# Kernel optimization log

Hardware: AMD Instinct MI355X
Metric: run time of the kernel (lower is better)

Reference implementation:

```python
import jax, jax.numpy as jnp
import numpy as np

B, N, L, H = 32, 1024, 512, 8  # batch, num_id, Input_len, num_head
EPS = 1e-5


def _ln(x, g, b):
    m = jnp.mean(x, axis=-1, keepdims=True)
    v = jnp.mean((x - m) ** 2, axis=-1, keepdims=True)
    return (x - m) / jnp.sqrt(v + EPS) * g + b


def setup_inputs() -> dict:
    key = jax.random.key(0)
    ks = iter(jax.random.split(key, 40))
    w = lambda shape, s=0.02: jax.random.normal(next(ks), shape, jnp.float32) * s
    inp = {"x": jax.random.normal(next(ks), (B, N, L), jnp.float32)}
    for p in ("t", "c"):  # Time_de_att and cross_de_att params (conv1d k=1 -> [L,L])
        inp[f"{p}_Wq"] = w((L, L)); inp[f"{p}_bq"] = w((L,))
        inp[f"{p}_Wk"] = w((L, L)); inp[f"{p}_bk"] = w((L,))
        inp[f"{p}_Wv"] = w((L, L)); inp[f"{p}_bv"] = w((L,))
        inp[f"{p}_Wo"] = w((L, L, 1, H)); inp[f"{p}_bo"] = w((L,))  # Conv2d kernel (1,H)
        inp[f"{p}_g"] = jnp.ones((L,), jnp.float32); inp[f"{p}_b"] = jnp.zeros((L,), jnp.float32)
    inp["s_Wq"] = w((N, N)); inp["s_bq"] = w((N,))
    inp["s_Wk"] = w((N, N)); inp["s_bk"] = w((N,))
    inp["s_Wv"] = w((N, N)); inp["s_bv"] = w((N,))
    inp["s_W1"] = w((1, H)); inp["s_b1"] = w((1,))
    return inp


def _conv1x1(x_cn, W, b):  # x_cn: [B,C,len], W: [O,C]
    return jnp.einsum('oc,bcn->bon', W, x_cn) + b[None, :, None]


def _de_att(xq_src, xkv_src, Wq, bq, Wk, bk, Wv, bv, Wo, bo, g, bt):
    # xq_src, xkv_src: [B,L,N] (channels-first, as after x.transpose(-2,-1))
    q = _conv1x1(xq_src, Wq, bq).transpose(0, 2, 1)   # [B,N,L]
    k = _conv1x1(xkv_src, Wk, bk)                     # [B,L,N]
    v = _conv1x1(xkv_src, Wv, bv).transpose(0, 2, 1)  # [B,N,L]
    kd = jnp.sqrt(jnp.float32(N) / H)                 # k.shape[-1] == num_id
    attn = jax.nn.softmax(jnp.matmul(q, k) / kd, axis=-1)  # [B,N,N]
    line = jnp.matmul(attn, v)                        # [B,N,L]
    # eval-mode: all heads identical -> Conv2d(1,H) combine == sum weights over head axis
    Wsum = Wo[:, :, 0, :].sum(-1)                     # [L,L]
    res = jnp.einsum('oc,bcn->bon', Wsum, line.transpose(0, 2, 1)) + bo[None, :, None]
    out = (xkv_src + res).transpose(0, 2, 1)          # [B,N,L]
    return _ln(out, g, bt)


def reference(x,
              t_Wq, t_bq, t_Wk, t_bk, t_Wv, t_bv, t_Wo, t_bo, t_g, t_b,
              c_Wq, c_bq, c_Wk, c_bk, c_Wv, c_bv, c_Wo, c_bo, c_g, c_b,
              s_Wq, s_bq, s_Wk, s_bk, s_Wv, s_bv, s_W1, s_b1):
    xt = x.transpose(0, 2, 1)  # [B,L,N]
    # Time_de_att (self-attention over nodes, time as channels)
    time_out = _de_att(xt, xt, t_Wq, t_bq, t_Wk, t_bk, t_Wv, t_bv, t_Wo, t_bo, t_g, t_b)  # [B,N,L]
    # space_att2 (attention over time, nodes as features)
    q = xt @ s_Wq.T + s_bq                          # [B,L,N]
    k = (xt @ s_Wk.T + s_bk).transpose(0, 2, 1)     # [B,N,L]
    v = xt @ s_Wv.T + s_bv                          # [B,L,N]
    kd = jnp.sqrt(jnp.float32(L) / H)               # k.shape[-1] == Input_len
    line = jnp.matmul(jax.nn.softmax(jnp.matmul(q, k) / kd, axis=-1), v)  # [B,L,N]
    space_out = (line * s_W1.sum() + s_b1[0]).transpose(0, 2, 1)          # [B,N,L]
    # cross_de_att: q from space_out, k/v + residual from time_out
    out = _de_att(space_out.transpose(0, 2, 1), time_out.transpose(0, 2, 1),
                  c_Wq, c_bq, c_Wk, c_bk, c_Wv, c_bv, c_Wo, c_bo, c_g, c_b)
    return out  # [B,N,L]
```

## Files before the change

kernel.cpp:

```cpp
#include <hip/hip_runtime.h>
#include <hip/hip_bf16.h>

typedef __bf16 bf16;
typedef __bf16 bf16x8 __attribute__((ext_vector_type(8)));
typedef __bf16 bf16x4 __attribute__((ext_vector_type(4)));
typedef __bf16 bf16x2 __attribute__((ext_vector_type(2)));
typedef float f32x4 __attribute__((ext_vector_type(4)));

#define BATCH 32
#define N_ID 1024
#define L_IN 512

static const long ACT_E = (long)BATCH * N_ID * L_IN;
static const long S_NL  = (long)N_ID * L_IN;
static const long S_TT  = (long)N_ID * N_ID;

__device__ __forceinline__ void gload16(const bf16* g, bf16* l)
{
    __builtin_amdgcn_global_load_lds((__attribute__((address_space(1))) void*)g,
                                     (__attribute__((address_space(3))) void*)l, 16, 0, 0);
}

#define VM8 asm volatile("s_waitcnt vmcnt(8)" ::: "memory")
#define VM4 asm volatile("s_waitcnt vmcnt(4)" ::: "memory")
#define VM0 asm volatile("s_waitcnt vmcnt(0)" ::: "memory")
#define BAR __builtin_amdgcn_s_barrier()

#define COMPUTE(CIDX) \
    { \
      const bf16* pa = ldsb + (CIDX) * 8192; \
      const bf16* pb = pa + 4096; \
      bf16x8 af[4], bfv[4]; \
_Pragma("unroll") \
      for (int i = 0; i < 4; ++i) \
        af[i] = *(const bf16x8*)(pa + (wm * 64 + i * 16 + fr) * 32 + slotk); \
_Pragma("unroll") \
      for (int j = 0; j < 4; ++j) \
        bfv[j] = *(const bf16x8*)(pb + (wn * 64 + j * 16 + fr) * 32 + slotk); \
      __builtin_amdgcn_s_setprio(1); \
_Pragma("unroll") \
      for (int i = 0; i < 4; ++i) \
_Pragma("unroll") \
        for (int j = 0; j < 4; ++j) \
          acc[i][j] = __builtin_amdgcn_mfma_f32_16x16x32_bf16(af[i], bfv[j], acc[i][j], 0, 0, 0); \
      __builtin_amdgcn_s_setprio(0); \
    }

#define STAGE(CIDX, KT) { stg(ldsb + (CIDX) * 8192, Ab, lda, m0, KT); \
                          stg(ldsb + (CIDX) * 8192 + 4096, Bb, ldb, n0, KT); }

template<int EPI>
__global__ __launch_bounds__(256, 3)
void gemm3(const bf16* __restrict__ A, const bf16* __restrict__ Bm, void* __restrict__ Cout,
           const float* __restrict__ biasCol, const float* __restrict__ biasRow,
           const void* __restrict__ Res, const float* __restrict__ scal2,
           float scale, int K,
           long lda, long ldb, long ldc,
           long sA, long sB, long sC, long sRes, long sBR,
           unsigned gy, unsigned gxy, unsigned nwg)
{
    __shared__ __align__(16) bf16 ldsbuf[3 * 2 * 4096];
    bf16* ldsb = ldsbuf;

    unsigned id = blockIdx.x;
    {
        const unsigned q = nwg >> 3, r = nwg & 7;
        const unsigned xcd = id & 7, off = id >> 3;
        id = (xcd < r ? xcd * (q + 1) : r * (q + 1) + (xcd - r) * q) + off;
    }
    const unsigned bz = id / gxy;
    const unsigned rem = id - bz * gxy;
    const unsigned bx = rem / gy;
    const unsigned by = rem - bx * gy;

    const int t = threadIdx.x;
    const int w = t >> 6;
    const int lane = t & 63;
    const int fr = lane & 15;
    const int kg = lane >> 4;
    const int wm = w >> 1, wn = w & 1;
    const long z = bz;
    const long m0 = (long)bx * 128;
    const long n0 = (long)by * 128;
    const bf16* Ab = A + z * sA;
    const bf16* Bb = Bm + z * sB;

    const int srow = w * 16 + (lane >> 2);
    const int gc = (lane & 3) ^ ((lane >> 3) & 3);
    const int slotk = (kg ^ ((fr >> 1) & 3)) * 8;

    auto stg = [&](bf16* dst, const bf16* base, long ld, long rc0, int kt) {
#pragma unroll
        for (int r = 0; r < 2; ++r) {
            const int row = r * 64 + srow;
            const bf16* src = base + (rc0 + row) * ld + kt * 32 + gc * 8;
            gload16(src, dst + row * 32 + (lane & 3) * 8);
        }
    };

    f32x4 acc[4][4] = {};

    const int NT = K >> 5;
    STAGE(0, 0); STAGE(1, 1); STAGE(2, 2);

    int c = 0;
    for (int kt = 0; kt < NT - 2; ++kt) {
        VM8; BAR;
        COMPUTE(c);
        BAR;
        if (kt + 3 < NT) STAGE(c, kt + 3);
        c = (c == 2) ? 0 : c + 1;
    }
    VM4; BAR;
    COMPUTE(c);
    BAR;
    c = (c == 2) ? 0 : c + 1;
    VM0; BAR;
    COMPUTE(c);

    float e0 = 0.f, e1 = 0.f;
    if constexpr (EPI == 8) { e0 = scal2[0]; e1 = scal2[1]; }

    float rs[16];
    if constexpr (EPI == 6) {
#pragma unroll
        for (int vv = 0; vv < 16; ++vv) rs[vv] = 0.f;
    }

#pragma unroll
    for (int i = 0; i < 4; ++i) {
        const long rb = m0 + wm * 64 + i * 16 + kg * 4;
        float rin[4];
        if constexpr (EPI == 7) {
#pragma unroll
            for (int r = 0; r < 4; ++r) rin[r] = 1.f / biasRow[z * sBR + rb + r];
        }
#pragma unroll
        for (int j = 0; j < 4; ++j) {
            const long cc = n0 + wn * 64 + j * 16 + fr;
            float cinv = 0.f, vj = 0.f;
            if constexpr (EPI == 8) cinv = 1.f / biasCol[z * sBR + cc];
            if constexpr (EPI == 6) vj = biasCol[z * sBR + cc];
#pragma unroll
            for (int r = 0; r < 4; ++r) {
                const long rr = rb + r;
                const float v = acc[i][j][r];
                const long idx = z * sC + rr * ldc + cc;
                if constexpr (EPI == 1)      ((bf16*)Cout)[idx] = (bf16)(v + biasRow[rr]);
                else if constexpr (EPI == 3) ((bf16*)Cout)[idx] = (bf16)v;
                else if constexpr (EPI == 6) {
                    const float e = __builtin_amdgcn_exp2f(v * scale + vj);
                    ((bf16*)Cout)[idx] = (bf16)e;
                    rs[i * 4 + r] += e;
                }
                else if constexpr (EPI == 7) ((bf16*)Cout)[idx] =
                    (bf16)(v * rin[r]
                           + (float)((const bf16*)Res)[z * sRes + rr * ldc + cc] + biasCol[cc]);
                else                  ((bf16*)Cout)[idx] = (bf16)(v * cinv * e0 + e1);
            }
        }
    }

    if constexpr (EPI == 6) {
#pragma unroll
        for (int vv = 0; vv < 16; ++vv) {
            rs[vv] += __shfl_xor(rs[vv], 1);
            rs[vv] += __shfl_xor(rs[vv], 2);
            rs[vv] += __shfl_xor(rs[vv], 4);
            rs[vv] += __shfl_xor(rs[vv], 8);
        }
        if (fr == 0) {
            float* Rs = (float*)biasRow + z * sBR;
#pragma unroll
            for (int i = 0; i < 4; ++i)
#pragma unroll
                for (int r = 0; r < 4; ++r) {
                    const long rr = m0 + wm * 64 + i * 16 + kg * 4 + r;
                    atomicAdd(Rs + rr, rs[i * 4 + r]);
                }
        }
    }
}

template<int OUTBF>
__global__ __launch_bounds__(128)
void ln_rows(const bf16* __restrict__ X, const float* __restrict__ g,
             const float* __restrict__ bta, void* __restrict__ out)
{
    const long row = blockIdx.x;
    const int t = threadIdx.x;
    bf16x4 b4 = *(const bf16x4*)(X + row * 512 + t * 4);
    float v[4] = { (float)b4[0], (float)b4[1], (float)b4[2], (float)b4[3] };
    float s1 = v[0] + v[1] + v[2] + v[3];
    float s2 = v[0]*v[0] + v[1]*v[1] + v[2]*v[2] + v[3]*v[3];
#pragma unroll
    for (int o = 32; o > 0; o >>= 1) { s1 += __shfl_xor(s1, o); s2 += __shfl_xor(s2, o); }
    __shared__ float r1[2], r2[2];
    const int w = t >> 6, l = t & 63;
    if (l == 0) { r1[w] = s1; r2[w] = s2; }
    __syncthreads();
    s1 = r1[0] + r1[1];
    s2 = r2[0] + r2[1];
    const float mean = s1 * (1.f / 512.f);
    const float var  = s2 * (1.f / 512.f) - mean * mean;
    const float rstd = rsqrtf(var + 1e-5f);
    const int c = t * 4;
    if constexpr (OUTBF) {
        bf16x4 o4;
#pragma unroll
        for (int k = 0; k < 4; ++k) o4[k] = (bf16)((v[k] - mean) * rstd * g[c + k] + bta[c + k]);
        *(bf16x4*)((bf16*)out + row * 512 + c) = o4;
    } else {
        f32x4 o4;
#pragma unroll
        for (int k = 0; k < 4; ++k) o4[k] = (v[k] - mean) * rstd * g[c + k] + bta[c + k];
        *(f32x4*)((float*)out + row * 512 + c) = o4;
    }
}

__global__ __launch_bounds__(256)
void transpose_cvt(const float* __restrict__ x, bf16* __restrict__ Xb, bf16* __restrict__ xt)
{
    __shared__ bf16 tile[32][33];
    const int b = blockIdx.z;
    const int n0 = blockIdx.x * 32, l0 = blockIdx.y * 32;
    const long base = (long)b * N_ID * L_IN;
    const int tx = threadIdx.x, ty = threadIdx.y;
#pragma unroll
    for (int i = ty; i < 32; i += 8) {
        const long idx = base + (long)(n0 + i) * L_IN + l0 + tx;
        const bf16 s = (bf16)x[idx];
        Xb[idx] = s;
        tile[i][tx] = s;
    }
    __syncthreads();
#pragma unroll
    for (int i = ty; i < 32; i += 8)
        xt[base + (long)(l0 + i) * N_ID + n0 + tx] = tile[tx][i];
}

template<int N>
__global__ __launch_bounds__(256)
void transpose_mat(const float* __restrict__ a, const float* __restrict__ b,
                   bf16* __restrict__ da, bf16* __restrict__ db)
{
    __shared__ bf16 tile[32][33];
    const float* src = blockIdx.z ? b : a;
    bf16* dst = blockIdx.z ? db : da;
    const int c0 = blockIdx.x * 32, r0 = blockIdx.y * 32;
    const int tx = threadIdx.x, ty = threadIdx.y;
#pragma unroll
    for (int i = ty; i < 32; i += 8)
        tile[i][tx] = (bf16)src[(long)(r0 + i) * N + c0 + tx];
    __syncthreads();
#pragma unroll
    for (int i = ty; i < 32; i += 8)
        dst[(long)(c0 + i) * N + r0 + tx] = tile[tx][i];
}

__global__ void cvt_one(const float* __restrict__ s, bf16* __restrict__ d, int n)
{
    const int i = (blockIdx.x * 256 + threadIdx.x) * 4;
    if (i < n) {
        f32x4 v = *(const f32x4*)(s + i);
        bf16x4 o; o[0] = (bf16)v[0]; o[1] = (bf16)v[1]; o[2] = (bf16)v[2]; o[3] = (bf16)v[3];
        *(bf16x4*)(d + i) = o;
    }
}

__global__ void wo_sum2(const float* __restrict__ a, const float* __restrict__ b,
                        bf16* __restrict__ da, bf16* __restrict__ db)
{
    const int i = blockIdx.x * 256 + threadIdx.x;
    const float* src = blockIdx.y ? b : a;
    bf16* dst = blockIdx.y ? db : da;
    const float* p = src + (long)i * 8;
    float s = 0.f;
#pragma unroll
    for (int h = 0; h < 8; ++h) s += p[h];
    dst[i] = (bf16)s;
}

__global__ __launch_bounds__(64)
void biasfold2(const bf16* __restrict__ WsA, const float* __restrict__ bvA, const float* __restrict__ boA, float* __restrict__ outA,
               const bf16* __restrict__ WsB, const float* __restrict__ bvB, const float* __restrict__ boB, float* __restrict__ outB)
{
    const bf16* Ws = blockIdx.y ? WsB : WsA;
    const float* bv = blockIdx.y ? bvB : bvA;
    const float* bo = blockIdx.y ? boB : boA;
    float* out = blockIdx.y ? outB : outA;
    const int o = blockIdx.x;
    float s = 0.f;
    for (int l = threadIdx.x; l < 512; l += 64)
        s += (float)Ws[(long)o * 512 + l] * bv[l];
#pragma unroll
    for (int off = 32; off > 0; off >>= 1) s += __shfl_xor(s, off);
    if (threadIdx.x == 0) out[o] = bo[o] + s;
}

__global__ __launch_bounds__(64)
void vbarfold(const bf16* WkTrT, const float* tbq, float* vbarT,
              const bf16* WkTrC, const float* cbq, float* vbarC,
              const bf16* sWkTr, const float* sbq, float* vbarS,
              const float* sW1, const float* sb1, float* scal)
{
    const int o = blockIdx.x;
    const int y = blockIdx.y;
    if (y == 3) {
        if (o == 0 && threadIdx.x == 0) {
            float s = 0.f;
            for (int h = 0; h < 8; ++h) s += sW1[h];
            scal[0] = s; scal[1] = sb1[0];
        }
        return;
    }
    const bf16* W; const float* b; float* out; int D;
    if (y == 0)      { if (o >= 512) return; W = WkTrT; b = tbq; out = vbarT; D = 512; }
    else if (y == 1) { if (o >= 512) return; W = WkTrC; b = cbq; out = vbarC; D = 512; }
    else             { W = sWkTr; b = sbq; out = vbarS; D = 1024; }
    float s = 0.f;
    for (int a = threadIdx.x; a < D; a += 64)
        s += (float)W[(long)o * D + a] * b[a];
#pragma unroll
    for (int off = 32; off > 0; off >>= 1) s += __shfl_xor(s, off);
    if (threadIdx.x == 0) out[o] = s;
}

template<int D>
__global__ __launch_bounds__(256)
void vrow(const bf16* __restrict__ Src, const float* __restrict__ vbar,
          float* __restrict__ out, float scale2)
{
    const long row = (long)blockIdx.x * 4 + (threadIdx.x >> 6);
    const int lane = threadIdx.x & 63;
    const bf16* r = Src + row * D;
    float s = 0.f;
#pragma unroll
    for (int u = 0; u < D / 512; ++u) {
        bf16x8 xv = *(const bf16x8*)(r + u * 512 + lane * 8);
        const float* vb = vbar + u * 512 + lane * 8;
#pragma unroll
        for (int e = 0; e < 8; ++e) s += (float)xv[e] * vb[e];
    }
#pragma unroll
    for (int o = 32; o > 0; o >>= 1) s += __shfl_xor(s, o);
    if (lane == 0) out[row] = s * scale2;
}

static void launch_gemm(int epi, const bf16* A, const bf16* B, void* C,
                        const float* bc, const float* br, const void* res, const float* sc2,
                        float scale, int M, int N, int K,
                        long lda, long ldb, long ldc,
                        long sA, long sB, long sC, long sRes, long sBR,
                        int batches, hipStream_t st)
{
    const unsigned gx = M / 128, gy = N / 128;
    const unsigned gxy = gx * gy, nwg = gxy * (unsigned)batches;
    dim3 g(nwg), blk(256);
    switch (epi) {
    case 1: gemm3<1><<<g, blk, 0, st>>>(A, B, C, bc, br, res, sc2, scale, K, lda, ldb, ldc, sA, sB, sC, sRes, sBR, gy, gxy, nwg); break;
    case 3: gemm3<3><<<g, blk, 0, st>>>(A, B, C, bc, br, res, sc2, scale, K, lda, ldb, ldc, sA, sB, sC, sRes, sBR, gy, gxy, nwg); break;
    case 6: gemm3<6><<<g, blk, 0, st>>>(A, B, C, bc, br, res, sc2, scale, K, lda, ldb, ldc, sA, sB, sC, sRes, sBR, gy, gxy, nwg); break;
    case 7: gemm3<7><<<g, blk, 0, st>>>(A, B, C, bc, br, res, sc2, scale, K, lda, ldb, ldc, sA, sB, sC, sRes, sBR, gy, gxy, nwg); break;
    default: gemm3<8><<<g, blk, 0, st>>>(A, B, C, bc, br, res, sc2, scale, K, lda, ldb, ldc, sA, sB, sC, sRes, sBR, gy, gxy, nwg); break;
    }
}

extern "C" void kernel_launch(void* const* d_in, const int* in_sizes, int n_in,
                              void* d_out, int out_size, void* d_ws, size_t ws_size,
                              hipStream_t stream)
{
    (void)in_sizes; (void)n_in; (void)out_size;

    const float* x   = (const float*)d_in[0];
    const float* tWq = (const float*)d_in[1];  const float* tbq = (const float*)d_in[2];
    const float* tWk = (const float*)d_in[3];  const float* tbk = (const float*)d_in[4];
    const float* tWv = (const float*)d_in[5];  const float* tbv = (const float*)d_in[6];
    const float* tWo = (const float*)d_in[7];  const float* tbo = (const float*)d_in[8];
    const float* tg  = (const float*)d_in[9];  const float* tb  = (const float*)d_in[10];
    const float* cWq = (const float*)d_in[11]; const float* cbq = (const float*)d_in[12];
    const float* cWk = (const float*)d_in[13]; const float* cbk = (const float*)d_in[14];
    const float* cWv = (const float*)d_in[15]; const float* cbv = (const float*)d_in[16];
    const float* cWo = (const float*)d_in[17]; const float* cbo = (const float*)d_in[18];
    const float* cg  = (const float*)d_in[19]; const float* cb  = (const float*)d_in[20];
    const float* sWq = (const float*)d_in[21]; const float* sbq = (const float*)d_in[22];
    const float* sWk = (const float*)d_in[23]; const float* sbk = (const float*)d_in[24];
    const float* sWv = (const float*)d_in[25]; const float* sbv = (const float*)d_in[26];
    const float* sW1 = (const float*)d_in[27]; const float* sb1 = (const float*)d_in[28];
    (void)tbk; (void)cbk; (void)sbk;

    char* p = (char*)d_ws;
    auto alloc = [&](size_t bytes) -> char* {
        char* r = p; p += (bytes + 255) & ~(size_t)255; return r;
    };

    bf16* WsT   = (bf16*)alloc(262144 * 2);
    bf16* WsC   = (bf16*)alloc(262144 * 2);
    bf16* WkTrT = (bf16*)alloc(262144 * 2);
    bf16* WkTrC = (bf16*)alloc(262144 * 2);
    bf16* WvTrT = (bf16*)alloc(262144 * 2);
    bf16* WvTrC = (bf16*)alloc(262144 * 2);
    bf16* WqTrT = (bf16*)alloc(262144 * 2);
    bf16* WqTrC = (bf16*)alloc(262144 * 2);
    bf16* WvWT  = (bf16*)alloc(262144 * 2);
    bf16* WvWC  = (bf16*)alloc(262144 * 2);
    bf16* MTt   = (bf16*)alloc(262144 * 2);
    bf16* MTc   = (bf16*)alloc(262144 * 2);
    bf16* sWqTr = (bf16*)alloc(1048576 * 2);
    bf16* sWkTr = (bf16*)alloc(1048576 * 2);
    bf16* MTs   = (bf16*)alloc(1048576 * 2);
    bf16* WvS   = (bf16*)alloc(1048576 * 2);
    float* scal  = (float*)alloc(256);
    float* biasT = (float*)alloc(512 * 4);
    float* biasC = (float*)alloc(512 * 4);
    float* vbarT = (float*)alloc(512 * 4);
    float* vbarC = (float*)alloc(512 * 4);
    float* vbarS = (float*)alloc(1024 * 4);

    const size_t ACT_B = (size_t)ACT_E * 2;
    bf16* bufG = (bf16*)alloc(ACT_B);
    bf16* Xb   = (bf16*)alloc(ACT_B);
    bf16* TO   = (bf16*)alloc(ACT_B);
    bf16* xt   = (bf16*)alloc(ACT_B);
    bf16* bufV = (bf16*)alloc(ACT_B);
    bf16* PL   = (bf16*)alloc(ACT_B);
    float* vpre = (float*)alloc(BATCH * 1024 * 4);
    float* Rbuf = (float*)alloc(BATCH * 1024 * 4);

    size_t used = (size_t)(p - (char*)d_ws);
    int CB = 32;
    while (CB > 1 && used + (size_t)CB * 2097152ULL + 4096 > ws_size) CB >>= 1;
    bf16* Sbuf = (bf16*)alloc((size_t)CB * 2097152ULL);
    bf16* Pbuf = Sbuf;

    const float L2E = 1.4426950408889634f;
    const float rsc_t2 = 0.08838834764831845f * L2E;
    const float rsc_s2 = 0.125f * L2E;

    transpose_mat<512><<<dim3(16, 16, 2), dim3(32, 8), 0, stream>>>(tWv, cWv, WvTrT, WvTrC);
    transpose_mat<512><<<dim3(16, 16, 2), dim3(32, 8), 0, stream>>>(tWq, cWq, WqTrT, WqTrC);
    transpose_mat<512><<<dim3(16, 16, 2), dim3(32, 8), 0, stream>>>(tWk, cWk, WkTrT, WkTrC);
    transpose_mat<1024><<<dim3(32, 32, 2), dim3(32, 8), 0, stream>>>(sWq, sWk, sWqTr, sWkTr);
    cvt_one<<<dim3(1024), dim3(256), 0, stream>>>(sWv, WvS, 1048576);
    wo_sum2<<<dim3(1024, 2), dim3(256), 0, stream>>>(tWo, cWo, WsT, WsC);
    biasfold2<<<dim3(512, 2), dim3(64), 0, stream>>>(WsT, tbv, tbo, biasT, WsC, cbv, cbo, biasC);
    vbarfold<<<dim3(1024, 4), dim3(64), 0, stream>>>(WkTrT, tbq, vbarT, WkTrC, cbq, vbarC,
                                                     sWkTr, sbq, vbarS, sW1, sb1, scal);
    launch_gemm(3, WsT, WvTrT, WvWT, nullptr, nullptr, nullptr, nullptr, 0.f,
                512, 512, 512, 512, 512, 512, 262144, 262144, 262144, 0, 0, 4, stream);
    launch_gemm(3, sWkTr, sWqTr, MTs, nullptr, nullptr, nullptr, nullptr, 0.f,
                1024, 1024, 1024, 1024, 1024, 1024, 0, 0, 0, 0, 0, 1, stream);
    transpose_cvt<<<dim3(32, 16, BATCH), dim3(32, 8), 0, stream>>>(x, Xb, xt);

    auto attn_tc = [&](const bf16* Kb, const bf16* ResP, const float* biasP) {
        for (int c0 = 0; c0 < BATCH; c0 += CB) {
            const long off = (long)c0 * S_NL;
            hipMemsetAsync(Rbuf, 0, (size_t)CB * 1024 * 4, stream);
            launch_gemm(6, bufG + off, Kb + off, Sbuf, vpre + (long)c0 * 1024, Rbuf, nullptr, nullptr, rsc_t2,
                        1024, 1024, 512, 512, 512, 1024, S_NL, S_NL, S_TT, 0, 1024, CB, stream);
            launch_gemm(7, Pbuf, bufV + off, PL + off, biasP, Rbuf, ResP + off, nullptr, 0.f,
                        1024, 512, 1024, 1024, 1024, 512, S_TT, S_NL, S_NL, S_NL, 1024, CB, stream);
        }
    };

    launch_gemm(3, Xb, MTt, bufG, nullptr, nullptr, nullptr, nullptr, 0.f,
                32768, 512, 512, 512, 512, 512, 0, 0, 0, 0, 0, 1, stream);
    launch_gemm(3, WvWT, Xb, bufV, nullptr, nullptr, nullptr, nullptr, 0.f,
                512, 1024, 512, 512, 512, 1024, 0, S_NL, S_NL, 0, 0, BATCH, stream);
    vrow<512><<<dim3(8192), dim3(256), 0, stream>>>(Xb, vbarT, vpre, rsc_t2);
    attn_tc(Xb, Xb, biasT);
    ln_rows<1><<<dim3(32768), dim3(128), 0, stream>>>(PL, tg, tb, TO);

    bf16* SOp = Xb;
    launch_gemm(3, xt, MTs, bufG, nullptr, nullptr, nullptr, nullptr, 0.f,
                16384, 1024, 1024, 1024, 1024, 1024, 0, 0, 0, 0, 0, 1, stream);
    launch_gemm(1, WvS, xt, bufV, nullptr, sbv, nullptr, nullptr, 0.f,
                1024, 512, 1024, 1024, 1024, 512, 0, S_NL, S_NL, 0, 0, BATCH, stream);
    vrow<1024><<<dim3(4096), dim3(256), 0, stream>>>(xt, vbarS, vpre, rsc_s2);
    for (int c0 = 0; c0 < BATCH; c0 += CB) {
        const long off = (long)c0 * S_NL;
        hipMemsetAsync(Rbuf, 0, (size_t)CB * 512 * 4, stream);
        launch_gemm(6, bufG + off, xt + off, Sbuf, vpre + (long)c0 * 512, Rbuf, nullptr, nullptr, rsc_s2,
                    512, 512, 1024, 1024, 1024, 512, S_NL, S_NL, (long)L_IN * L_IN, 0, 512, CB, stream);
        launch_gemm(8, bufV + off, Pbuf, SOp + off, Rbuf, nullptr, nullptr, scal, 0.f,
                    1024, 512, 512, 512, 512, 512, S_NL, (long)L_IN * L_IN, S_NL, 0, 512, CB, stream);
    }

    launch_gemm(3, Xb, MTc, bufG, nullptr, nullptr, nullptr, nullptr, 0.f,
                32768, 512, 512, 512, 512, 512, 0, 0, 0, 0, 0, 1, stream);
    launch_gemm(3, WvWC, TO, bufV, nullptr, nullptr, nullptr, nullptr, 0.f,
                512, 1024, 512, 512, 512, 1024, 0, S_NL, S_NL, 0, 0, BATCH, stream);
    vrow<512><<<dim3(8192), dim3(256), 0, stream>>>(TO, vbarC, vpre, rsc_t2);
    attn_tc(TO, TO, biasC);
    ln_rows<0><<<dim3(32768), dim3(128), 0, stream>>>(PL, cg, cb, d_out);
}
```

Baseline: 649.9 us.

## Double-buffer GEMM for occupancy, replace atomic row sums with slot partials, batch small kernels

The GEMM pipeline drops from three LDS stages to two so that four workgroups can fit per CU instead of three. The softmax row-sum accumulation now writes per-tile partial sums into slot buffers instead of using atomics, and the consumer epilogues reduce those slots. This removes the memsets and atomic contention. The three weight transposes are merged into one launch, and LayerNorm now handles two rows per block. The shallower pipeline exposes more memory latency per workgroup, and the consumers do extra loads to reduce the partials.

```diff
diff --git a/kernel.cpp b/kernel.cpp
--- a/kernel.cpp
+++ b/kernel.cpp
@@ -21,7 +21,6 @@
                                      (__attribute__((address_space(3))) void*)l, 16, 0, 0);
 }
 
-#define VM8 asm volatile("s_waitcnt vmcnt(8)" ::: "memory")
 #define VM4 asm volatile("s_waitcnt vmcnt(4)" ::: "memory")
 #define VM0 asm volatile("s_waitcnt vmcnt(0)" ::: "memory")
 #define BAR __builtin_amdgcn_s_barrier()
@@ -50,16 +49,16 @@
                           stg(ldsb + (CIDX) * 8192 + 4096, Bb, ldb, n0, KT); }
 
 template<int EPI>
-__global__ __launch_bounds__(256, 3)
+__global__ __launch_bounds__(256, 4)
 void gemm3(const bf16* __restrict__ A, const bf16* __restrict__ Bm, void* __restrict__ Cout,
            const float* __restrict__ biasCol, const float* __restrict__ biasRow,
            const void* __restrict__ Res, const float* __restrict__ scal2,
            float scale, int K,
            long lda, long ldb, long ldc,
-           long sA, long sB, long sC, long sRes, long sBR,
+           long sA, long sB, long sC, long sRes, long sBR, long sVp, int nsl,
            unsigned gy, unsigned gxy, unsigned nwg)
 {
-    __shared__ __align__(16) bf16 ldsbuf[3 * 2 * 4096];
+    __shared__ __align__(16) bf16 ldsbuf[2 * 2 * 4096];
     bf16* ldsb = ldsbuf;
 
     unsigned id = blockIdx.x;
@@ -101,22 +100,16 @@
     f32x4 acc[4][4] = {};
 
     const int NT = K >> 5;
-    STAGE(0, 0); STAGE(1, 1); STAGE(2, 2);
-
-    int c = 0;
-    for (int kt = 0; kt < NT - 2; ++kt) {
-        VM8; BAR;
-        COMPUTE(c);
+    STAGE(0, 0); STAGE(1, 1);
+
+    for (int kt = 0; kt < NT - 1; ++kt) {
+        VM4; BAR;
+        COMPUTE(kt & 1);
         BAR;
-        if (kt + 3 < NT) STAGE(c, kt + 3);
-        c = (c == 2) ? 0 : c + 1;
-    }
-    VM4; BAR;
-    COMPUTE(c);
-    BAR;
-    c = (c == 2) ? 0 : c + 1;
+        if (kt + 2 < NT) STAGE(kt & 1, kt + 2);
+    }
     VM0; BAR;
-    COMPUTE(c);
+    COMPUTE((NT - 1) & 1);
 
     float e0 = 0.f, e1 = 0.f;
     if constexpr (EPI == 8) { e0 = scal2[0]; e1 = scal2[1]; }
@@ -133,14 +126,24 @@
         float rin[4];
         if constexpr (EPI == 7) {
 #pragma unroll
-            for (int r = 0; r < 4; ++r) rin[r] = 1.f / biasRow[z * sBR + rb + r];
+            for (int r = 0; r < 4; ++r) {
+                float s = biasRow[z * sBR + (rb + r) * 16 + fr];
+                s += __shfl_xor(s, 1); s += __shfl_xor(s, 2);
+                s += __shfl_xor(s, 4); s += __shfl_xor(s, 8);
+                rin[r] = 1.f / s;
+            }
         }
 #pragma unroll
         for (int j = 0; j < 4; ++j) {
             const long cc = n0 + wn * 64 + j * 16 + fr;
             float cinv = 0.f, vj = 0.f;
-            if constexpr (EPI == 8) cinv = 1.f / biasCol[z * sBR + cc];
-            if constexpr (EPI == 6) vj = biasCol[z * sBR + cc];
+            if constexpr (EPI == 8) {
+                float s = 0.f;
+#pragma unroll
+                for (int k8 = 0; k8 < 8; ++k8) s += biasCol[z * sBR + cc * 8 + k8];
+                cinv = 1.f / s;
+            }
+            if constexpr (EPI == 6) vj = biasCol[z * sVp + cc];
 #pragma unroll
             for (int r = 0; r < 4; ++r) {
                 const long rr = rb + r;
@@ -171,40 +174,42 @@
         }
         if (fr == 0) {
             float* Rs = (float*)biasRow + z * sBR;
+            const int slot = (int)by * 2 + wn;
 #pragma unroll
             for (int i = 0; i < 4; ++i)
 #pragma unroll
                 for (int r = 0; r < 4; ++r) {
                     const long rr = m0 + wm * 64 + i * 16 + kg * 4 + r;
-                    atomicAdd(Rs + rr, rs[i * 4 + r]);
+                    Rs[rr * nsl + slot] = rs[i * 4 + r];
                 }
         }
     }
 }
 
 template<int OUTBF>
-__global__ __launch_bounds__(128)
+__global__ __launch_bounds__(256)
 void ln_rows(const bf16* __restrict__ X, const float* __restrict__ g,
              const float* __restrict__ bta, void* __restrict__ out)
 {
-    const long row = blockIdx.x;
-    const int t = threadIdx.x;
-    bf16x4 b4 = *(const bf16x4*)(X + row * 512 + t * 4);
+    const int rloc = threadIdx.x >> 7;
+    const int t2 = threadIdx.x & 127;
+    const long row = (long)blockIdx.x * 2 + rloc;
+    bf16x4 b4 = *(const bf16x4*)(X + row * 512 + t2 * 4);
     float v[4] = { (float)b4[0], (float)b4[1], (float)b4[2], (float)b4[3] };
     float s1 = v[0] + v[1] + v[2] + v[3];
     float s2 = v[0]*v[0] + v[1]*v[1] + v[2]*v[2] + v[3]*v[3];
 #pragma unroll
     for (int o = 32; o > 0; o >>= 1) { s1 += __shfl_xor(s1, o); s2 += __shfl_xor(s2, o); }
-    __shared__ float r1[2], r2[2];
-    const int w = t >> 6, l = t & 63;
-    if (l == 0) { r1[w] = s1; r2[w] = s2; }
+    __shared__ float r1[2][2], r2[2][2];
+    const int w = t2 >> 6, l = t2 & 63;
+    if (l == 0) { r1[rloc][w] = s1; r2[rloc][w] = s2; }
     __syncthreads();
-    s1 = r1[0] + r1[1];
-    s2 = r2[0] + r2[1];
+    s1 = r1[rloc][0] + r1[rloc][1];
+    s2 = r2[rloc][0] + r2[rloc][1];
     const float mean = s1 * (1.f / 512.f);
     const float var  = s2 * (1.f / 512.f) - mean * mean;
     const float rstd = rsqrtf(var + 1e-5f);
-    const int c = t * 4;
+    const int c = t2 * 4;
     if constexpr (OUTBF) {
         bf16x4 o4;
 #pragma unroll
@@ -237,6 +242,25 @@
 #pragma unroll
     for (int i = ty; i < 32; i += 8)
         xt[base + (long)(l0 + i) * N_ID + n0 + tx] = tile[tx][i];
+}
+
+struct T6 { const float* s[6]; bf16* d[6]; };
+
+__global__ __launch_bounds__(256)
+void transpose512_6(T6 p)
+{
+    __shared__ bf16 tile[32][33];
+    const float* src = p.s[blockIdx.z];
+    bf16* dst = p.d[blockIdx.z];
+    const int c0 = blockIdx.x * 32, r0 = blockIdx.y * 32;
+    const int tx = threadIdx.x, ty = threadIdx.y;
+#pragma unroll
+    for (int i = ty; i < 32; i += 8)
+        tile[i][tx] = (bf16)src[(long)(r0 + i) * 512 + c0 + tx];
+    __syncthreads();
+#pragma unroll
+    for (int i = ty; i < 32; i += 8)
+        dst[(long)(c0 + i) * 512 + r0 + tx] = tile[tx][i];
 }
 
 template<int N>
@@ -351,18 +375,18 @@
                         const float* bc, const float* br, const void* res, const float* sc2,
                         float scale, int M, int N, int K,
                         long lda, long ldb, long ldc,
-                        long sA, long sB, long sC, long sRes, long sBR,
+                        long sA, long sB, long sC, long sRes, long sBR, long sVp, int nsl,
                         int batches, hipStream_t st)
 {
     const unsigned gx = M / 128, gy = N / 128;
     const unsigned gxy = gx * gy, nwg = gxy * (unsigned)batches;
     dim3 g(nwg), blk(256);
     switch (epi) {
-    case 1: gemm3<1><<<g, blk, 0, st>>>(A, B, C, bc, br, res, sc2, scale, K, lda, ldb, ldc, sA, sB, sC, sRes, sBR, gy, gxy, nwg); break;
-    case 3: gemm3<3><<<g, blk, 0, st>>>(A, B, C, bc, br, res, sc2, scale, K, lda, ldb, ldc, sA, sB, sC, sRes, sBR, gy, gxy, nwg); break;
-    case 6: gemm3<6><<<g, blk, 0, st>>>(A, B, C, bc, br, res, sc2, scale, K, lda, ldb, ldc, sA, sB, sC, sRes, sBR, gy, gxy, nwg); break;
-    case 7: gemm3<7><<<g, blk, 0, st>>>(A, B, C, bc, br, res, sc2, scale, K, lda, ldb, ldc, sA, sB, sC, sRes, sBR, gy, gxy, nwg); break;
-    default: gemm3<8><<<g, blk, 0, st>>>(A, B, C, bc, br, res, sc2, scale, K, lda, ldb, ldc, sA, sB, sC, sRes, sBR, gy, gxy, nwg); break;
+    case 1: gemm3<1><<<g, blk, 0, st>>>(A, B, C, bc, br, res, sc2, scale, K, lda, ldb, ldc, sA, sB, sC, sRes, sBR, sVp, nsl, gy, gxy, nwg); break;
+    case 3: gemm3<3><<<g, blk, 0, st>>>(A, B, C, bc, br, res, sc2, scale, K, lda, ldb, ldc, sA, sB, sC, sRes, sBR, sVp, nsl, gy, gxy, nwg); break;
+    case 6: gemm3<6><<<g, blk, 0, st>>>(A, B, C, bc, br, res, sc2, scale, K, lda, ldb, ldc, sA, sB, sC, sRes, sBR, sVp, nsl, gy, gxy, nwg); break;
+    case 7: gemm3<7><<<g, blk, 0, st>>>(A, B, C, bc, br, res, sc2, scale, K, lda, ldb, ldc, sA, sB, sC, sRes, sBR, sVp, nsl, gy, gxy, nwg); break;
+    default: gemm3<8><<<g, blk, 0, st>>>(A, B, C, bc, br, res, sc2, scale, K, lda, ldb, ldc, sA, sB, sC, sRes, sBR, sVp, nsl, gy, gxy, nwg); break;
     }
 }
 
@@ -374,20 +398,19 @@
 
     const float* x   = (const float*)d_in[0];
     const float* tWq = (const float*)d_in[1];  const float* tbq = (const float*)d_in[2];
-    const float* tWk = (const float*)d_in[3];  const float* tbk = (const float*)d_in[4];
+    const float* tWk = (const float*)d_in[3];
     const float* tWv = (const float*)d_in[5];  const float* tbv = (const float*)d_in[6];
     const float* tWo = (const float*)d_in[7];  const float* tbo = (const float*)d_in[8];
     const float* tg  = (const float*)d_in[9];  const float* tb  = (const float*)d_in[10];
     const float* cWq = (const float*)d_in[11]; const float* cbq = (const float*)d_in[12];
-    const float* cWk = (const float*)d_in[13]; const float* cbk = (const float*)d_in[14];
+    const float* cWk = (const float*)d_in[13];
     const float* cWv = (const float*)d_in[15]; const float* cbv = (const float*)d_in[16];
     const float* cWo = (const float*)d_in[17]; const float* cbo = (const float*)d_in[18];
     const float* cg  = (const float*)d_in[19]; const float* cb  = (const float*)d_in[20];
     const float* sWq = (const float*)d_in[21]; const float* sbq = (const float*)d_in[22];
-    const float* sWk = (const float*)d_in[23]; const float* sbk = (const float*)d_in[24];
+    const float* sWk = (const float*)d_in[23];
     const float* sWv = (const float*)d_in[25]; const float* sbv = (const float*)d_in[26];
     const float* sW1 = (const float*)d_in[27]; const float* sb1 = (const float*)d_in[28];
-    (void)tbk; (void)cbk; (void)sbk;
 
     char* p = (char*)d_ws;
     auto alloc = [&](size_t bytes) -> char* {
@@ -425,7 +448,7 @@
     bf16* bufV = (bf16*)alloc(ACT_B);
     bf16* PL   = (bf16*)alloc(ACT_B);
     float* vpre = (float*)alloc(BATCH * 1024 * 4);
-    float* Rbuf = (float*)alloc(BATCH * 1024 * 4);
+    float* Rbuf = (float*)alloc((size_t)BATCH * 1024 * 16 * 4);
 
     size_t used = (size_t)(p - (char*)d_ws);
     int CB = 32;
@@ -437,9 +460,10 @@
     const float rsc_t2 = 0.08838834764831845f * L2E;
     const float rsc_s2 = 0.125f * L2E;
 
-    transpose_mat<512><<<dim3(16, 16, 2), dim3(32, 8), 0, stream>>>(tWv, cWv, WvTrT, WvTrC);
-    transpose_mat<512><<<dim3(16, 16, 2), dim3(32, 8), 0, stream>>>(tWq, cWq, WqTrT, WqTrC);
-    transpose_mat<512><<<dim3(16, 16, 2), dim3(32, 8), 0, stream>>>(tWk, cWk, WkTrT, WkTrC);
+    T6 tj;
+    tj.s[0] = tWv; tj.s[1] = cWv; tj.s[2] = tWq; tj.s[3] = cWq; tj.s[4] = tWk; tj.s[5] = cWk;
+    tj.d[0] = WvTrT; tj.d[1] = WvTrC; tj.d[2] = WqTrT; tj.d[3] = WqTrC; tj.d[4] = WkTrT; tj.d[5] = WkTrC;
+    transpose512_6<<<dim3(16, 16, 6), dim3(32, 8), 0, stream>>>(tj);
     transpose_mat<1024><<<dim3(32, 32, 2), dim3(32, 8), 0, stream>>>(sWq, sWk, sWqTr, sWkTr);
     cvt_one<<<dim3(1024), dim3(256), 0, stream>>>(sWv, WvS, 1048576);
     wo_sum2<<<dim3(1024, 2), dim3(256), 0, stream>>>(tWo, cWo, WsT, WsC);
@@ -447,50 +471,48 @@
     vbarfold<<<dim3(1024, 4), dim3(64), 0, stream>>>(WkTrT, tbq, vbarT, WkTrC, cbq, vbarC,
                                                      sWkTr, sbq, vbarS, sW1, sb1, scal);
     launch_gemm(3, WsT, WvTrT, WvWT, nullptr, nullptr, nullptr, nullptr, 0.f,
-                512, 512, 512, 512, 512, 512, 262144, 262144, 262144, 0, 0, 4, stream);
+                512, 512, 512, 512, 512, 512, 262144, 262144, 262144, 0, 0, 0, 0, 4, stream);
     launch_gemm(3, sWkTr, sWqTr, MTs, nullptr, nullptr, nullptr, nullptr, 0.f,
-                1024, 1024, 1024, 1024, 1024, 1024, 0, 0, 0, 0, 0, 1, stream);
+                1024, 1024, 1024, 1024, 1024, 1024, 0, 0, 0, 0, 0, 0, 0, 1, stream);
     transpose_cvt<<<dim3(32, 16, BATCH), dim3(32, 8), 0, stream>>>(x, Xb, xt);
 
     auto attn_tc = [&](const bf16* Kb, const bf16* ResP, const float* biasP) {
         for (int c0 = 0; c0 < BATCH; c0 += CB) {
             const long off = (long)c0 * S_NL;
-            hipMemsetAsync(Rbuf, 0, (size_t)CB * 1024 * 4, stream);
             launch_gemm(6, bufG + off, Kb + off, Sbuf, vpre + (long)c0 * 1024, Rbuf, nullptr, nullptr, rsc_t2,
-                        1024, 1024, 512, 512, 512, 1024, S_NL, S_NL, S_TT, 0, 1024, CB, stream);
+                        1024, 1024, 512, 512, 512, 1024, S_NL, S_NL, S_TT, 0, 16384, 1024, 16, CB, stream);
             launch_gemm(7, Pbuf, bufV + off, PL + off, biasP, Rbuf, ResP + off, nullptr, 0.f,
-                        1024, 512, 1024, 1024, 1024, 512, S_TT, S_NL, S_NL, S_NL, 1024, CB, stream);
+                        1024, 512, 1024, 1024, 1024, 512, S_TT, S_NL, S_NL, S_NL, 16384, 0, 16, CB, stream);
         }
     };
 
     launch_gemm(3, Xb, MTt, bufG, nullptr, nullptr, nullptr, nullptr, 0.f,
-                32768, 512, 512, 512, 512, 512, 0, 0, 0, 0, 0, 1, stream);
+                32768, 512, 512, 512, 512, 512, 0, 0, 0, 0, 0, 0, 0, 1, stream);
     launch_gemm(3, WvWT, Xb, bufV, nullptr, nullptr, nullptr, nullptr, 0.f,
-                512, 1024, 512, 512, 512, 1024, 0, S_NL, S_NL, 0, 0, BATCH, stream);
+                512, 1024, 512, 512, 512, 1024, 0, S_NL, S_NL, 0, 0, 0, 0, BATCH, stream);
     vrow<512><<<dim3(8192), dim3(256), 0, stream>>>(Xb, vbarT, vpre, rsc_t2);
     attn_tc(Xb, Xb, biasT);
-    ln_rows<1><<<dim3(32768), dim3(128), 0, stream>>>(PL, tg, tb, TO);
+    ln_rows<1><<<dim3(16384), dim3(256), 0, stream>>>(PL, tg, tb, TO);
 
     bf16* SOp = Xb;
     launch_gemm(3, xt, MTs, bufG, nullptr, nullptr, nullptr, nullptr, 0.f,
-                16384, 1024, 1024, 1024, 1024, 1024, 0, 0, 0, 0, 0, 1, stream);
+                16384, 1024, 1024, 1024, 1024, 1024, 0, 0, 0, 0, 0, 0, 0, 1, stream);
     launch_gemm(1, WvS, xt, bufV, nullptr, sbv, nullptr, nullptr, 0.f,
-                1024, 512, 1024, 1024, 1024, 512, 0, S_NL, S_NL, 0, 0, BATCH, stream);
+                1024, 512, 1024, 1024, 1024, 512, 0, S_NL, S_NL, 0, 0, 0, 0, BATCH, stream);
     vrow<1024><<<dim3(4096), dim3(256), 0, stream>>>(xt, vbarS, vpre, rsc_s2);
     for (int c0 = 0; c0 < BATCH; c0 += CB) {
         const long off = (long)c0 * S_NL;
-        hipMemsetAsync(Rbuf, 0, (size_t)CB * 512 * 4, stream);
         launch_gemm(6, bufG + off, xt + off, Sbuf, vpre + (long)c0 * 512, Rbuf, nullptr, nullptr, rsc_s2,
-                    512, 512, 1024, 1024, 1024, 512, S_NL, S_NL, (long)L_IN * L_IN, 0, 512, CB, stream);
+                    512, 512, 1024, 1024, 1024, 512, S_NL, S_NL, (long)L_IN * L_IN, 0, 4096, 512, 8, CB, stream);
         launch_gemm(8, bufV + off, Pbuf, SOp + off, Rbuf, nullptr, nullptr, scal, 0.f,
-                    1024, 512, 512, 512, 512, 512, S_NL, (long)L_IN * L_IN, S_NL, 0, 512, CB, stream);
+                    1024, 512, 512, 512, 512, 512, S_NL, (long)L_IN * L_IN, S_NL, 0, 4096, 0, 8, CB, stream);
     }
 
     launch_gemm(3, Xb, MTc, bufG, nullptr, nullptr, nullptr, nullptr, 0.f,
-                32768, 512, 512, 512, 512, 512, 0, 0, 0, 0, 0, 1, stream);
+                32768, 512, 512, 512, 512, 512, 0, 0, 0, 0, 0, 0, 0, 1, stream);
     launch_gemm(3, WvWC, TO, bufV, nullptr, nullptr, nullptr, nullptr, 0.f,
-                512, 1024, 512, 512, 512, 1024, 0, S_NL, S_NL, 0, 0, BATCH, stream);
+                512, 1024, 512, 512, 512, 1024, 0, S_NL, S_NL, 0, 0, 0, 0, BATCH, stream);
     vrow<512><<<dim3(8192), dim3(256), 0, stream>>>(TO, vbarC, vpre, rsc_t2);
     attn_tc(TO, TO, biasC);
-    ln_rows<0><<<dim3(32768), dim3(128), 0, stream>>>(PL, cg, cb, d_out);
-}
+    ln_rows<0><<<dim3(16384), dim3(256), 0, stream>>>(PL, cg, cb, d_out);
+}
```

Measured after the change: 652.5 us. No clear change (+0.4%).
